# Kernel tuning notes

Measured on AMD Instinct MI355X. Metric: run time of the kernel, lower is better.

The kernel has to match this reference:

```python
import jax, jax.numpy as jnp
import numpy as np

N_NODES = 131072          # total nodes across all expressions
NODES_PER_EXPR = 64       # nodes per expression (left or right side)
NUM_SEG = N_NODES // NODES_PER_EXPR   # 2048 segments = 1024 equations x 2 sides
VOCAB = 320
D_MODEL = 128
NUM_LAYERS = 4


def setup_inputs() -> dict:
    key = jax.random.key(0)
    ks = jax.random.split(key, 8)
    # combined-vocab index per node (leaf->token id, internal->function id + offset)
    node_idx = jax.random.randint(ks[0], (N_NODES,), 0, VOCAB)
    # 4 incoming edges per node: left child, right child, parent, self.
    # index N_NODES is the padding node (zero features).
    nb = jax.random.randint(ks[1], (N_NODES, 3), 0, N_NODES + 1)
    self_col = jnp.arange(N_NODES)[:, None]
    neighbors = jnp.concatenate([nb, self_col], axis=1)  # [N, 4]
    # contiguous expression segments (matches batched DGL graph layout)
    seg_ids = jnp.arange(N_NODES) // NODES_PER_EXPR
    emb = jax.random.normal(ks[2], (VOCAB, D_MODEL), dtype=jnp.float32) * 0.02
    W0 = jax.random.normal(ks[3], (NUM_LAYERS, 4 * D_MODEL, D_MODEL), dtype=jnp.float32) * (1.0 / np.sqrt(4 * D_MODEL))
    b0 = jnp.zeros((NUM_LAYERS, D_MODEL), dtype=jnp.float32)
    W1 = jax.random.normal(ks[4], (NUM_LAYERS, D_MODEL, D_MODEL), dtype=jnp.float32) * (1.0 / np.sqrt(D_MODEL))
    b1 = jnp.zeros((NUM_LAYERS, D_MODEL), dtype=jnp.float32)
    out_bias = jnp.zeros((1,), dtype=jnp.float32)
    return {"node_idx": node_idx, "neighbors": neighbors, "seg_ids": seg_ids,
            "emb": emb, "W0": W0, "b0": b0, "W1": W1, "b1": b1, "out_bias": out_bias}


def reference(node_idx, neighbors, seg_ids, emb, W0, b0, W1, b1, out_bias):
    N, d = node_idx.shape[0], emb.shape[1]
    feats = emb[node_idx]                                   # [N, d] embedding lookup
    num_layers = W0.shape[0]
    for l in range(num_layers):
        # padding node (id N) always contributes zero features
        f_pad = jnp.concatenate([feats, jnp.zeros((1, d), feats.dtype)], axis=0)
        gathered = f_pad[neighbors].reshape(N, 4 * d)       # [N, 4d] mailbox gather+flatten
        h = jax.nn.relu(gathered @ W0[l] + b0[l])           # FunctionModule layer 1
        feats = h @ W1[l] + b1[l]                           # FunctionModule layer 2
    # per-expression mean feature (graph readout)
    sums = jax.ops.segment_sum(feats, seg_ids, num_segments=NUM_SEG)      # [2B, d]
    cnts = jax.ops.segment_sum(jnp.ones((N,), feats.dtype), seg_ids, num_segments=NUM_SEG)
    means = sums / cnts[:, None]
    means = means.reshape(-1, 2, d)                         # [B, 2, d] (left, right)
    logits = jnp.einsum('bd,bd->b', means[:, 0], means[:, 1]) + out_bias[0]
    return logits
```

## Files before the change

### kernel.cpp

```cpp
#include <hip/hip_runtime.h>

#define N_NODES 131072
#define D 128
#define NLAYERS 4
#define VOCAB 320

typedef _Float16 f16;
typedef _Float16 f16x8 __attribute__((ext_vector_type(8)));
typedef float f32x4 __attribute__((ext_vector_type(4)));
typedef unsigned int u32;

__global__ __launch_bounds__(256) void prep_wf(
    const float* __restrict__ W0, const float* __restrict__ W1,
    f16* __restrict__ W0f, f16* __restrict__ W1f,
    f16* __restrict__ fa, f16* __restrict__ fb)
{
    const int b = blockIdx.x, tid = threadIdx.x;
    if (b == 1280) {
        if (tid < 32) {
            f16x8 z = {0, 0, 0, 0, 0, 0, 0, 0};
            f16* base = (tid >> 4) ? fb : fa;
            *(f16x8*)&base[(size_t)N_NODES * D + (tid & 15) * 8] = z;
        }
        return;
    }
    if (b < 1024) {
        int i = b * 256 + tid;
        int l = i >> 16, r = i & 65535;
        int k = r >> 7, n = r & 127;
        int e = k >> 7, t = (k >> 5) & 3, q = (k >> 3) & 3, j = k & 7;
        int g = n >> 4, lm = n & 15;
        int o = ((e * 4 + t) * 8 + g) * 512 + q * 128 + lm * 8 + j;
        W0f[(size_t)l * 65536 + o] = (f16)W0[i];
    } else {
        int i = (b - 1024) * 256 + tid;
        int l = i >> 14, r = i & 16383;
        int k = r >> 7, n = r & 127;
        int t = k >> 5, q = (k >> 3) & 3, j = k & 7;
        int g = n >> 4, lm = n & 15;
        int o = (t * 8 + g) * 512 + q * 128 + lm * 8 + j;
        W1f[(size_t)l * 16384 + o] = (f16)W1[i];
    }
}

__global__ __launch_bounds__(256) void prep_emb(
    const float* __restrict__ emb, f16* __restrict__ embP)
{
    const int tid = threadIdx.x;
    if (blockIdx.x == 40) {
        if (tid < 16) {
            f16x8 z = {0, 0, 0, 0, 0, 0, 0, 0};
            *(f16x8*)&embP[(size_t)VOCAB * D + tid * 8] = z;
        }
        return;
    }
    int i = blockIdx.x * 256 + tid;
    int t = i >> 5, c = i & 31;
    float4 x = ((const float4*)emb)[(size_t)t * 32 + c];
    f16 v[4] = {(f16)x.x, (f16)x.y, (f16)x.z, (f16)x.w};
    *(unsigned long long*)&embP[(size_t)t * D + c * 4] = *(unsigned long long*)v;
}

__global__ __launch_bounds__(256) void prep_nbrtok(
    const int* __restrict__ node_idx, const int* __restrict__ neighbors,
    int* __restrict__ nbr_tok)
{
    int i = blockIdx.x * 256 + threadIdx.x;
    int nbr = neighbors[i];
    nbr_tok[i] = (nbr < N_NODES) ? node_idx[nbr] : VOCAB;
}

#define NID4(v, e) ((e) == 0 ? (v).x : (e) == 1 ? (v).y : (e) == 2 ? (v).z : (v).w)
#define SLOAD(e_) {                                                          \
    _Pragma("unroll")                                                        \
    for (int i = 0; i < 4; ++i)                                              \
        sg[i] = *(const f16x8*)&fin[(size_t)NID4(rn4[i], e_) * D + kb * 8]; }
#define SSTORE(buf) {                                                        \
    _Pragma("unroll")                                                        \
    for (int i = 0; i < 4; ++i) {                                            \
        int row = r0 + 16 * i;                                               \
        *(f16x8*)&As[buf][row * 128 + ((kb ^ (row & 7)) * 8)] = sg[i];       \
    } }
#define LOAD_B(buf, s) {                                                     \
    _Pragma("unroll")                                                        \
    for (int c = 0; c < 2; ++c)                                              \
        bf[buf][c] = *(const f16x8*)&W0f[(size_t)((s) * 8 + w * 2 + c) * 512 + lane * 8]; }

template <bool FINAL>
__global__ __launch_bounds__(256, 4) void layer_k(
    const f16* __restrict__ fin, f16* __restrict__ fout,
    float* __restrict__ means, const int* __restrict__ nbrtab,
    const f16* __restrict__ W0f, const float* __restrict__ b0,
    const f16* __restrict__ W1f, const float* __restrict__ b1)
{
    __shared__ f16 As[2][64 * 128];

    const int tid  = threadIdx.x;
    const int bm   = blockIdx.x * 64;
    const int lane = tid & 63;
    const int w    = tid >> 6;
    const int quad = lane >> 4, lm = lane & 15;
    const int kb   = tid & 15;
    const int r0   = tid >> 4;

    int4 rn4[4];
#pragma unroll
    for (int i = 0; i < 4; ++i)
        rn4[i] = *(const int4*)&nbrtab[(size_t)(bm + r0 + 16 * i) * 4];

    float bb0[2], bb1[2];
#pragma unroll
    for (int c = 0; c < 2; ++c) {
        bb0[c] = b0[w * 32 + c * 16 + lm];
        bb1[c] = b1[w * 32 + c * 16 + lm];
    }

    f16x8 sg[4], bf[4][2];
    SLOAD(0)
    LOAD_B(0, 0)
    LOAD_B(1, 1)
    LOAD_B(2, 2)
    SSTORE(0)
    __syncthreads();

    f32x4 acc1[4][2];
#pragma unroll
    for (int r = 0; r < 4; ++r)
#pragma unroll
        for (int c = 0; c < 2; ++c) acc1[r][c] = (f32x4){0.f, 0.f, 0.f, 0.f};

#pragma unroll
    for (int e = 0; e < 4; ++e) {
        if (e < 3) SLOAD(e + 1)
#pragma unroll
        for (int t = 0; t < 4; ++t) {
            const int s = e * 4 + t;
            if (s < 13) LOAD_B((s + 3) & 3, s + 3)
            f16x8 af[4];
#pragma unroll
            for (int r = 0; r < 4; ++r) {
                int row = r * 16 + lm;
                af[r] = *(const f16x8*)&As[e & 1][row * 128 + (((t * 4 + quad) ^ (lm & 7)) * 8)];
            }
#pragma unroll
            for (int r = 0; r < 4; ++r)
#pragma unroll
                for (int c = 0; c < 2; ++c)
                    acc1[r][c] = __builtin_amdgcn_mfma_f32_16x16x32_f16(
                        af[r], bf[s & 3][c], acc1[r][c], 0, 0, 0);
        }
        if (e < 3) {
            SSTORE((e + 1) & 1)
            __syncthreads();
        }
    }

    unsigned int hpk[4][2][2];
#pragma unroll
    for (int c = 0; c < 2; ++c)
#pragma unroll
        for (int r = 0; r < 4; ++r)
#pragma unroll
            for (int p = 0; p < 2; ++p) {
                float v0 = fmaxf(acc1[r][c][2 * p]     + bb0[c], 0.f);
                float v1 = fmaxf(acc1[r][c][2 * p + 1] + bb0[c], 0.f);
                unsigned short u0 = __builtin_bit_cast(unsigned short, (f16)v0);
                unsigned short u1 = __builtin_bit_cast(unsigned short, (f16)v1);
                hpk[r][c][p] = ((u32)u1 << 16) | u0;
            }

#pragma unroll
    for (int r = 0; r < 4; ++r)
#pragma unroll
        for (int c = 0; c < 2; ++c) {
            int gcol = w * 32 + c * 16 + lm;
            int blk = gcol >> 3, el = gcol & 7;
#pragma unroll
            for (int reg = 0; reg < 4; ++reg) {
                int grow = r * 16 + quad * 4 + reg;
                unsigned pk = hpk[r][c][reg >> 1];
                unsigned short bits = (reg & 1) ? (unsigned short)(pk >> 16)
                                                : (unsigned short)(pk & 0xffff);
                As[0][grow * 128 + ((blk ^ (grow & 7)) * 8) + el] =
                    __builtin_bit_cast(f16, bits);
            }
        }

    f16x8 pbf[4][2];
#pragma unroll
    for (int t = 0; t < 4; ++t)
#pragma unroll
        for (int c = 0; c < 2; ++c)
            pbf[t][c] = *(const f16x8*)&W1f[(size_t)(t * 8 + w * 2 + c) * 512 + lane * 8];
    __syncthreads();

    f32x4 acc2[4][2];
#pragma unroll
    for (int r = 0; r < 4; ++r)
#pragma unroll
        for (int c = 0; c < 2; ++c) acc2[r][c] = (f32x4){0.f, 0.f, 0.f, 0.f};

#pragma unroll
    for (int t = 0; t < 4; ++t) {
        f16x8 a2[4];
#pragma unroll
        for (int r = 0; r < 4; ++r) {
            int row = r * 16 + lm;
            a2[r] = *(const f16x8*)&As[0][row * 128 + (((4 * t + quad) ^ (lm & 7)) * 8)];
        }
#pragma unroll
        for (int r = 0; r < 4; ++r)
#pragma unroll
            for (int c = 0; c < 2; ++c)
                acc2[r][c] = __builtin_amdgcn_mfma_f32_16x16x32_f16(
                    a2[r], pbf[t][c], acc2[r][c], 0, 0, 0);
    }

    if (FINAL) {
#pragma unroll
        for (int c = 0; c < 2; ++c) {
            float pc = 0.f;
#pragma unroll
            for (int r = 0; r < 4; ++r)
#pragma unroll
                for (int reg = 0; reg < 4; ++reg) pc += acc2[r][c][reg];
            pc += __shfl_xor(pc, 16);
            pc += __shfl_xor(pc, 32);
            if (quad == 0)
                means[(size_t)blockIdx.x * 128 + w * 32 + c * 16 + lm] =
                    pc * (1.0f / 64.0f) + bb1[c];
        }
        return;
    }

    __syncthreads();
#pragma unroll
    for (int r = 0; r < 4; ++r)
#pragma unroll
        for (int c = 0; c < 2; ++c) {
            int gcol = w * 32 + c * 16 + lm;
            int blk = gcol >> 3, el = gcol & 7;
#pragma unroll
            for (int reg = 0; reg < 4; ++reg) {
                int grow = r * 16 + quad * 4 + reg;
                As[1][grow * 128 + ((blk ^ (grow & 7)) * 8) + el] =
                    (f16)(acc2[r][c][reg] + bb1[c]);
            }
        }
    __syncthreads();
#pragma unroll
    for (int i = 0; i < 4; ++i) {
        int row = r0 + 16 * i;
        *(f16x8*)&fout[(size_t)(bm + row) * D + kb * 8] =
            *(const f16x8*)&As[1][row * 128 + ((kb ^ (row & 7)) * 8)];
    }
}

__global__ __launch_bounds__(256) void dot_k(
    const float* __restrict__ means, const float* __restrict__ out_bias,
    float* __restrict__ logits)
{
    const int w    = (blockIdx.x << 2) + (threadIdx.x >> 6);
    const int lane = threadIdx.x & 63;
    const float2 a = *(const float2*)&means[(size_t)(2 * w) * 128 + lane * 2];
    const float2 b = *(const float2*)&means[(size_t)(2 * w + 1) * 128 + lane * 2];
    float v = a.x * b.x + a.y * b.y;
#pragma unroll
    for (int off = 32; off; off >>= 1) v += __shfl_down(v, off);
    if (lane == 0) logits[w] = v + out_bias[0];
}

extern "C" void kernel_launch(void* const* d_in, const int* in_sizes, int n_in,
                              void* d_out, int out_size, void* d_ws, size_t ws_size,
                              hipStream_t stream) {
    const int*   node_idx  = (const int*)d_in[0];
    const int*   neighbors = (const int*)d_in[1];
    const float* emb       = (const float*)d_in[3];
    const float* W0        = (const float*)d_in[4];
    const float* b0        = (const float*)d_in[5];
    const float* W1        = (const float*)d_in[6];
    const float* b1        = (const float*)d_in[7];
    const float* out_bias  = (const float*)d_in[8];
    float*       logits    = (float*)d_out;

    const size_t NP1 = (size_t)N_NODES + 1;
    f16*   feats_a = (f16*)d_ws;
    f16*   feats_b = feats_a + NP1 * D;
    f16*   W0f     = feats_b + NP1 * D;
    f16*   W1f     = W0f + (size_t)NLAYERS * 512 * 128;
    f16*   embP    = W1f + (size_t)NLAYERS * 128 * 128;
    int*   nbr_tok = (int*)(embP + (size_t)(VOCAB + 1) * D);
    float* means   = (float*)(nbr_tok + (size_t)N_NODES * 4);

    prep_wf<<<1281, 256, 0, stream>>>(W0, W1, W0f, W1f, feats_a, feats_b);
    prep_emb<<<41, 256, 0, stream>>>(emb, embP);
    prep_nbrtok<<<N_NODES * 4 / 256, 256, 0, stream>>>(node_idx, neighbors, nbr_tok);

    const int GRID = N_NODES / 64;

    layer_k<false><<<GRID, 256, 0, stream>>>(
        embP, feats_a, nullptr, nbr_tok, W0f, b0, W1f, b1);
    layer_k<false><<<GRID, 256, 0, stream>>>(
        feats_a, feats_b, nullptr, neighbors,
        W0f + (size_t)1 * 65536, b0 + 128, W1f + (size_t)1 * 16384, b1 + 128);
    layer_k<false><<<GRID, 256, 0, stream>>>(
        feats_b, feats_a, nullptr, neighbors,
        W0f + (size_t)2 * 65536, b0 + 256, W1f + (size_t)2 * 16384, b1 + 256);
    layer_k<true><<<GRID, 256, 0, stream>>>(
        feats_a, nullptr, means, neighbors,
        W0f + (size_t)3 * 65536, b0 + 384, W1f + (size_t)3 * 16384, b1 + 384);

    dot_k<<<256, 256, 0, stream>>>(means, out_bias, logits);
}
```

Before: 199.8 us.

## Deepen neighbor-gather prefetch to two stages and merge prep kernels

The layer kernel now keeps two register buffers of gathered neighbor rows, issuing global gathers two edge-slots ahead instead of one. This hides more of the random-access gather latency behind MFMA work. The three preprocessing kernels are folded into one launch to cut launch overhead. The extra register buffer raises VGPR pressure under the 4-blocks-per-SM launch bound, which could cause spills or lower occupancy.

```diff
diff --git a/kernel.cpp b/kernel.cpp
--- a/kernel.cpp
+++ b/kernel.cpp
@@ -10,20 +10,14 @@
 typedef float f32x4 __attribute__((ext_vector_type(4)));
 typedef unsigned int u32;
 
-__global__ __launch_bounds__(256) void prep_wf(
+__global__ __launch_bounds__(256) void prep_all(
     const float* __restrict__ W0, const float* __restrict__ W1,
-    f16* __restrict__ W0f, f16* __restrict__ W1f,
-    f16* __restrict__ fa, f16* __restrict__ fb)
+    const float* __restrict__ emb, const int* __restrict__ node_idx,
+    const int* __restrict__ neighbors,
+    f16* __restrict__ W0f, f16* __restrict__ W1f, f16* __restrict__ embP,
+    int* __restrict__ nbr_tok, f16* __restrict__ fa, f16* __restrict__ fb)
 {
     const int b = blockIdx.x, tid = threadIdx.x;
-    if (b == 1280) {
-        if (tid < 32) {
-            f16x8 z = {0, 0, 0, 0, 0, 0, 0, 0};
-            f16* base = (tid >> 4) ? fb : fa;
-            *(f16x8*)&base[(size_t)N_NODES * D + (tid & 15) * 8] = z;
-        }
-        return;
-    }
     if (b < 1024) {
         int i = b * 256 + tid;
         int l = i >> 16, r = i & 65535;
@@ -32,7 +26,7 @@
         int g = n >> 4, lm = n & 15;
         int o = ((e * 4 + t) * 8 + g) * 512 + q * 128 + lm * 8 + j;
         W0f[(size_t)l * 65536 + o] = (f16)W0[i];
-    } else {
+    } else if (b < 1280) {
         int i = (b - 1024) * 256 + tid;
         int l = i >> 14, r = i & 16383;
         int k = r >> 7, n = r & 127;
@@ -40,46 +34,42 @@
         int g = n >> 4, lm = n & 15;
         int o = (t * 8 + g) * 512 + q * 128 + lm * 8 + j;
         W1f[(size_t)l * 16384 + o] = (f16)W1[i];
+    } else if (b == 1280) {
+        if (tid < 32) {
+            f16x8 z = {0, 0, 0, 0, 0, 0, 0, 0};
+            f16* base = (tid >> 4) ? fb : fa;
+            *(f16x8*)&base[(size_t)N_NODES * D + (tid & 15) * 8] = z;
+        }
+    } else if (b < 1322) {
+        if (b == 1321) {
+            if (tid < 16) {
+                f16x8 z = {0, 0, 0, 0, 0, 0, 0, 0};
+                *(f16x8*)&embP[(size_t)VOCAB * D + tid * 8] = z;
+            }
+            return;
+        }
+        int i = (b - 1281) * 256 + tid;
+        int t = i >> 5, c = i & 31;
+        float4 x = ((const float4*)emb)[(size_t)t * 32 + c];
+        f16 v[4] = {(f16)x.x, (f16)x.y, (f16)x.z, (f16)x.w};
+        *(unsigned long long*)&embP[(size_t)t * D + c * 4] = *(unsigned long long*)v;
+    } else {
+        int i = (b - 1322) * 256 + tid;
+        int nbr = neighbors[i];
+        nbr_tok[i] = (nbr < N_NODES) ? node_idx[nbr] : VOCAB;
     }
 }
 
-__global__ __launch_bounds__(256) void prep_emb(
-    const float* __restrict__ emb, f16* __restrict__ embP)
-{
-    const int tid = threadIdx.x;
-    if (blockIdx.x == 40) {
-        if (tid < 16) {
-            f16x8 z = {0, 0, 0, 0, 0, 0, 0, 0};
-            *(f16x8*)&embP[(size_t)VOCAB * D + tid * 8] = z;
-        }
-        return;
-    }
-    int i = blockIdx.x * 256 + tid;
-    int t = i >> 5, c = i & 31;
-    float4 x = ((const float4*)emb)[(size_t)t * 32 + c];
-    f16 v[4] = {(f16)x.x, (f16)x.y, (f16)x.z, (f16)x.w};
-    *(unsigned long long*)&embP[(size_t)t * D + c * 4] = *(unsigned long long*)v;
-}
-
-__global__ __launch_bounds__(256) void prep_nbrtok(
-    const int* __restrict__ node_idx, const int* __restrict__ neighbors,
-    int* __restrict__ nbr_tok)
-{
-    int i = blockIdx.x * 256 + threadIdx.x;
-    int nbr = neighbors[i];
-    nbr_tok[i] = (nbr < N_NODES) ? node_idx[nbr] : VOCAB;
-}
-
 #define NID4(v, e) ((e) == 0 ? (v).x : (e) == 1 ? (v).y : (e) == 2 ? (v).z : (v).w)
-#define SLOAD(e_) {                                                          \
+#define SLOAD(buf, e_) {                                                     \
     _Pragma("unroll")                                                        \
     for (int i = 0; i < 4; ++i)                                              \
-        sg[i] = *(const f16x8*)&fin[(size_t)NID4(rn4[i], e_) * D + kb * 8]; }
-#define SSTORE(buf) {                                                        \
+        sg[buf][i] = *(const f16x8*)&fin[(size_t)NID4(rn4[i], e_) * D + kb * 8]; }
+#define SSTORE(buf, ab) {                                                    \
     _Pragma("unroll")                                                        \
     for (int i = 0; i < 4; ++i) {                                            \
         int row = r0 + 16 * i;                                               \
-        *(f16x8*)&As[buf][row * 128 + ((kb ^ (row & 7)) * 8)] = sg[i];       \
+        *(f16x8*)&As[ab][row * 128 + ((kb ^ (row & 7)) * 8)] = sg[buf][i];   \
     } }
 #define LOAD_B(buf, s) {                                                     \
     _Pragma("unroll")                                                        \
@@ -115,12 +105,13 @@
         bb1[c] = b1[w * 32 + c * 16 + lm];
     }
 
-    f16x8 sg[4], bf[4][2];
-    SLOAD(0)
+    f16x8 sg[2][4], bf[4][2];
+    SLOAD(0, 0)
+    SLOAD(1, 1)
     LOAD_B(0, 0)
     LOAD_B(1, 1)
     LOAD_B(2, 2)
-    SSTORE(0)
+    SSTORE(0, 0)
     __syncthreads();
 
     f32x4 acc1[4][2];
@@ -131,7 +122,7 @@
 
 #pragma unroll
     for (int e = 0; e < 4; ++e) {
-        if (e < 3) SLOAD(e + 1)
+        if (e < 2) SLOAD(e & 1, e + 2)
 #pragma unroll
         for (int t = 0; t < 4; ++t) {
             const int s = e * 4 + t;
@@ -150,7 +141,7 @@
                         af[r], bf[s & 3][c], acc1[r][c], 0, 0, 0);
         }
         if (e < 3) {
-            SSTORE((e + 1) & 1)
+            SSTORE((e + 1) & 1, (e + 1) & 1)
             __syncthreads();
         }
     }
@@ -292,9 +283,9 @@
     int*   nbr_tok = (int*)(embP + (size_t)(VOCAB + 1) * D);
     float* means   = (float*)(nbr_tok + (size_t)N_NODES * 4);
 
-    prep_wf<<<1281, 256, 0, stream>>>(W0, W1, W0f, W1f, feats_a, feats_b);
-    prep_emb<<<41, 256, 0, stream>>>(emb, embP);
-    prep_nbrtok<<<N_NODES * 4 / 256, 256, 0, stream>>>(node_idx, neighbors, nbr_tok);
+    prep_all<<<1322 + N_NODES * 4 / 256, 256, 0, stream>>>(
+        W0, W1, emb, node_idx, neighbors, W0f, W1f, embP, nbr_tok,
+        feats_a, feats_b);
 
     const int GRID = N_NODES / 64;
 
```

After: 198.6 us. No clear change (-0.6%).
